# Optimization experiments

Hardware: AMD Instinct MI355X
Metric: run time of the kernel (lower is better)

The kernel has to match this reference:

```python
import jax, jax.numpy as jnp
import numpy as np

B, S, HID = 1, 4096, 2048
H, KV, D = 16, 8, 128
EPS = 1e-6
ROPE_THETA = 10000.0


def _rms_norm(x, w, eps=EPS):
    # x: [..., D], normalize over last dim in fp32 like Qwen3 RMSNorm
    xf = x.astype(jnp.float32)
    var = jnp.mean(xf * xf, axis=-1, keepdims=True)
    return (xf * jax.lax.rsqrt(var + eps)).astype(x.dtype) * w


def _rotate_half(x):
    x1, x2 = jnp.split(x, 2, axis=-1)
    return jnp.concatenate([-x2, x1], axis=-1)


def setup_inputs() -> dict:
    key = jax.random.key(0)
    ks = jax.random.split(key, 6)
    hidden_states = jax.random.normal(ks[0], (B, S, HID), dtype=jnp.float32)
    wq = jax.random.normal(ks[1], (H * D, HID), dtype=jnp.float32) * 0.02
    wk = jax.random.normal(ks[2], (KV * D, HID), dtype=jnp.float32) * 0.02
    wv = jax.random.normal(ks[3], (KV * D, HID), dtype=jnp.float32) * 0.02
    wo = jax.random.normal(ks[4], (HID, H * D), dtype=jnp.float32) * 0.02
    q_norm_w = jnp.ones((D,), dtype=jnp.float32)
    k_norm_w = jnp.ones((D,), dtype=jnp.float32)
    # real rotary tables: inv_freq over half dim, duplicated (HF convention)
    inv_freq = 1.0 / (ROPE_THETA ** (jnp.arange(0, D, 2, dtype=jnp.float32) / D))
    pos = jnp.arange(S, dtype=jnp.float32)
    freqs = pos[:, None] * inv_freq[None, :]          # [S, D/2]
    emb = jnp.concatenate([freqs, freqs], axis=-1)    # [S, D]
    cos = jnp.cos(emb)[None].astype(jnp.float32)      # [B, S, D]
    sin = jnp.sin(emb)[None].astype(jnp.float32)
    return {"hidden_states": hidden_states, "cos": cos, "sin": sin,
            "wq": wq, "wk": wk, "wv": wv, "wo": wo,
            "q_norm_w": q_norm_w, "k_norm_w": k_norm_w}


def reference(hidden_states, cos, sin, wq, wk, wv, wo, q_norm_w, k_norm_w):
    b, s, _ = hidden_states.shape
    scaling = D ** -0.5
    # QKV projections (no bias), reshape to heads, QK RMSNorm, then [b, h, s, d]
    q = _rms_norm(jnp.einsum('bsh,oh->bso', hidden_states, wq).reshape(b, s, H, D), q_norm_w)
    k = _rms_norm(jnp.einsum('bsh,oh->bso', hidden_states, wk).reshape(b, s, KV, D), k_norm_w)
    v = jnp.einsum('bsh,oh->bso', hidden_states, wv).reshape(b, s, KV, D)
    q = q.transpose(0, 2, 1, 3)  # [b, H, s, d]
    k = k.transpose(0, 2, 1, 3)  # [b, KV, s, d]
    v = v.transpose(0, 2, 1, 3)
    # RoPE (cos/sin broadcast over head dim)
    c = cos[:, None, :, :]
    sn = sin[:, None, :, :]
    q = q * c + _rotate_half(q) * sn
    k = k * c + _rotate_half(k) * sn
    # GQA: repeat KV heads to H
    groups = H // KV
    k = jnp.repeat(k, groups, axis=1)
    v = jnp.repeat(v, groups, axis=1)
    # eager causal attention, softmax in fp32
    scores = jnp.einsum('bhqd,bhkd->bhqk', q, k) * scaling
    causal = jnp.tril(jnp.ones((s, s), dtype=bool))
    scores = jnp.where(causal[None, None], scores, jnp.finfo(jnp.float32).min)
    attn = jax.nn.softmax(scores.astype(jnp.float32), axis=-1).astype(q.dtype)
    out = jnp.einsum('bhqk,bhkd->bhqd', attn, v)
    out = out.transpose(0, 2, 1, 3).reshape(b, s, H * D)
    return jnp.einsum('bso,ho->bsh', out, wo)
```

## Files before the change

kernel.cpp:

```cpp
#include <hip/hip_runtime.h>
#include <hip/hip_bf16.h>

typedef __hip_bfloat16 bf16;
typedef __attribute__((ext_vector_type(8))) short short8;
typedef __attribute__((ext_vector_type(4))) float f32x4;

#define S_LEN 4096
#define HID_DIM 2048

#define QSCALE ((float)(0.08838834764831845 * 1.4426950408889634))

__device__ __forceinline__ void gld_lds16(const void* g, void* l) {
  __builtin_amdgcn_global_load_lds(
      (const __attribute__((address_space(1))) void*)g,
      (__attribute__((address_space(3))) void*)l, 16, 0, 0);
}

__device__ __forceinline__ float fexp2(float x) {
  return __builtin_amdgcn_exp2f(x);
}

template <int CTRL>
__device__ __forceinline__ float dppf(float x) {
  return __builtin_bit_cast(
      float, __builtin_amdgcn_update_dpp(0, __builtin_bit_cast(int, x), CTRL,
                                         0xf, 0xf, true));
}
__device__ __forceinline__ float rmax16(float x) {
  x = fmaxf(x, dppf<0xB1>(x));
  x = fmaxf(x, dppf<0x4E>(x));
  x = fmaxf(x, dppf<0x141>(x));
  x = fmaxf(x, dppf<0x140>(x));
  return x;
}
__device__ __forceinline__ float rsum16(float x) {
  x += dppf<0xB1>(x);
  x += dppf<0x4E>(x);
  x += dppf<0x141>(x);
  x += dppf<0x140>(x);
  return x;
}

__global__ __launch_bounds__(256) void k_cvt(const float* __restrict__ src,
                                             bf16* __restrict__ dst, int n) {
  long i = ((long)blockIdx.x * 256 + threadIdx.x) * 8;
  if (i >= n) return;
  float4 a = *reinterpret_cast<const float4*>(src + i);
  float4 b = *reinterpret_cast<const float4*>(src + i + 4);
  float v[8] = {a.x, a.y, a.z, a.w, b.x, b.y, b.z, b.w};
  short8 o;
#pragma unroll
  for (int j = 0; j < 8; ++j) {
    bf16 h = __float2bfloat16(v[j]);
    o[j] = *reinterpret_cast<short*>(&h);
  }
  *reinterpret_cast<short8*>(dst + i) = o;
}

template <typename OutT>
__global__ __launch_bounds__(512, 1) void k_gemm256(
    const bf16* __restrict__ A, const bf16* __restrict__ B,
    OutT* __restrict__ C, int M, int N, int K) {
  __shared__ bf16 Al[2][256 * 64];
  __shared__ bf16 Bl[2][256 * 64];
  const int tid = threadIdx.x;
  const int lane = tid & 63;
  const int wid = tid >> 6;
  const int wr = wid >> 2;
  const int wc = wid & 3;
  const long brow = (long)blockIdx.y * 256;
  const long bcol = (long)blockIdx.x * 256;
  const int NT = K >> 6;

  auto stage = [&](int kt, int buf) {
    const bf16* At = A + brow * K + kt * 64;
    const bf16* Bt = B + bcol * K + kt * 64;
#pragma unroll
    for (int i = 0; i < 4; ++i) {
      const int ch = tid + i * 512;
      const int row = ch >> 3;
      const int j = (ch & 7) ^ (row & 7);
      gld_lds16(At + (size_t)row * K + j * 8, &Al[buf][(wid * 64 + i * 512) * 8]);
    }
#pragma unroll
    for (int i = 0; i < 4; ++i) {
      const int ch = tid + i * 512;
      const int row = ch >> 3;
      const int j = (ch & 7) ^ (row & 7);
      gld_lds16(Bt + (size_t)row * K + j * 8, &Bl[buf][(wid * 64 + i * 512) * 8]);
    }
  };

  f32x4 acc0[4][4], acc1[4][4];
#pragma unroll
  for (int m = 0; m < 4; ++m)
#pragma unroll
    for (int n = 0; n < 4; ++n) {
      acc0[m][n] = (f32x4){0.f, 0.f, 0.f, 0.f};
      acc1[m][n] = (f32x4){0.f, 0.f, 0.f, 0.f};
    }

  const int l15 = lane & 15;
  const int cp0 = ((lane >> 4) ^ (lane & 7)) * 8;
  const int cp1 = ((4 + (lane >> 4)) ^ (lane & 7)) * 8;

  stage(0, 0);
  stage(1, 1);
  asm volatile("s_waitcnt vmcnt(8)" ::: "memory");
  __builtin_amdgcn_s_barrier();

  for (int kt = 0; kt < NT; ++kt) {
    const bf16* Ab = &Al[kt & 1][0];
    const bf16* Bb = &Bl[kt & 1][0];
    short8 bB[4][2], aA[4][2];
#pragma unroll
    for (int n = 0; n < 4; ++n) {
      const int rb = (wc * 64 + n * 16 + l15) * 64;
      bB[n][0] = *reinterpret_cast<const short8*>(&Bb[rb + cp0]);
      bB[n][1] = *reinterpret_cast<const short8*>(&Bb[rb + cp1]);
    }
#pragma unroll
    for (int m = 0; m < 4; ++m) {
      const int ra = (wr * 128 + m * 16 + l15) * 64;
      aA[m][0] = *reinterpret_cast<const short8*>(&Ab[ra + cp0]);
      aA[m][1] = *reinterpret_cast<const short8*>(&Ab[ra + cp1]);
    }
    __builtin_amdgcn_s_setprio(1);
#pragma unroll
    for (int m = 0; m < 4; ++m)
#pragma unroll
      for (int n = 0; n < 4; ++n) {
        acc0[m][n] = __builtin_amdgcn_mfma_f32_16x16x32_bf16(aA[m][0], bB[n][0],
                                                             acc0[m][n], 0, 0, 0);
        acc0[m][n] = __builtin_amdgcn_mfma_f32_16x16x32_bf16(aA[m][1], bB[n][1],
                                                             acc0[m][n], 0, 0, 0);
      }
    __builtin_amdgcn_s_setprio(0);
#pragma unroll
    for (int m = 0; m < 4; ++m) {
      const int ra = (wr * 128 + 64 + m * 16 + l15) * 64;
      aA[m][0] = *reinterpret_cast<const short8*>(&Ab[ra + cp0]);
      aA[m][1] = *reinterpret_cast<const short8*>(&Ab[ra + cp1]);
    }
    __builtin_amdgcn_s_setprio(1);
#pragma unroll
    for (int m = 0; m < 4; ++m)
#pragma unroll
      for (int n = 0; n < 4; ++n) {
        acc1[m][n] = __builtin_amdgcn_mfma_f32_16x16x32_bf16(aA[m][0], bB[n][0],
                                                             acc1[m][n], 0, 0, 0);
        acc1[m][n] = __builtin_amdgcn_mfma_f32_16x16x32_bf16(aA[m][1], bB[n][1],
                                                             acc1[m][n], 0, 0, 0);
      }
    __builtin_amdgcn_s_setprio(0);

    if (kt + 1 < NT) {
      __builtin_amdgcn_s_barrier();
      if (kt + 2 < NT) {
        stage(kt + 2, kt & 1);
        asm volatile("s_waitcnt vmcnt(8)" ::: "memory");
      } else {
        asm volatile("s_waitcnt vmcnt(0)" ::: "memory");
      }
      __builtin_amdgcn_s_barrier();
    }
  }

#pragma unroll
  for (int mh = 0; mh < 2; ++mh) {
#pragma unroll
    for (int m = 0; m < 4; ++m) {
      const long r0 = brow + wr * 128 + mh * 64 + m * 16 + (lane >> 4) * 4;
#pragma unroll
      for (int n = 0; n < 4; ++n) {
        const long c0 = bcol + wc * 64 + n * 16 + l15;
        const f32x4 v = mh ? acc1[m][n] : acc0[m][n];
#pragma unroll
        for (int r = 0; r < 4; ++r) {
          if constexpr (sizeof(OutT) == 2)
            C[(r0 + r) * N + c0] = __float2bfloat16(v[r]);
          else
            C[(r0 + r) * N + c0] = v[r];
        }
      }
    }
  }
}

template <typename OutT>
__global__ __launch_bounds__(256) void k_gemm_bt(
    const bf16* __restrict__ A, const bf16* __restrict__ B,
    OutT* __restrict__ C, int M, int N, int K) {
  __shared__ bf16 Al[2][128 * 32];
  __shared__ bf16 Bl[2][128 * 32];
  const int tid = threadIdx.x;
  const int lane = tid & 63;
  const int wid = tid >> 6;
  const int wr = wid >> 1;
  const int wc = wid & 1;
  const long brow = (long)blockIdx.y * 128;
  const long bcol = (long)blockIdx.x * 128;
  const int rsub = lane >> 2;
  const int ksub = (lane & 3) * 8;

  f32x4 acc[4][4];
#pragma unroll
  for (int i = 0; i < 4; ++i)
#pragma unroll
    for (int j = 0; j < 4; ++j) acc[i][j] = (f32x4){0.f, 0.f, 0.f, 0.f};

  const int NT = K >> 5;

  auto stage = [&](int buf, int kt) {
    const long k0 = (long)kt << 5;
#pragma unroll
    for (int ci = 0; ci < 2; ++ci) {
      const int c = wid + ci * 4;
      gld_lds16(A + (brow + c * 16 + rsub) * K + k0 + ksub, &Al[buf][c * 512]);
      gld_lds16(B + (bcol + c * 16 + rsub) * K + k0 + ksub, &Bl[buf][c * 512]);
    }
  };

  stage(0, 0);
  __syncthreads();

  const int arow = wr * 64 + (lane & 15);
  const int nrow = wc * 64 + (lane & 15);
  const int kk = (lane >> 4) * 8;

  for (int t = 0; t < NT; ++t) {
    const int buf = t & 1;
    if (t + 1 < NT) stage(buf ^ 1, t + 1);
    short8 af[4], bfr[4];
#pragma unroll
    for (int mt = 0; mt < 4; ++mt)
      af[mt] = *reinterpret_cast<const short8*>(&Al[buf][(arow + mt * 16) * 32 + kk]);
#pragma unroll
    for (int nt = 0; nt < 4; ++nt)
      bfr[nt] = *reinterpret_cast<const short8*>(&Bl[buf][(nrow + nt * 16) * 32 + kk]);
#pragma unroll
    for (int mt = 0; mt < 4; ++mt)
#pragma unroll
      for (int nt = 0; nt < 4; ++nt)
        acc[mt][nt] = __builtin_amdgcn_mfma_f32_16x16x32_bf16(af[mt], bfr[nt],
                                                              acc[mt][nt], 0, 0, 0);
    __syncthreads();
  }

#pragma unroll
  for (int mt = 0; mt < 4; ++mt) {
    const long r0 = brow + wr * 64 + mt * 16 + (lane >> 4) * 4;
#pragma unroll
    for (int nt = 0; nt < 4; ++nt) {
      const long c0 = bcol + wc * 64 + nt * 16 + (lane & 15);
#pragma unroll
      for (int r = 0; r < 4; ++r) {
        if constexpr (sizeof(OutT) == 2)
          C[(r0 + r) * N + c0] = __float2bfloat16(acc[mt][nt][r]);
        else
          C[(r0 + r) * N + c0] = acc[mt][nt][r];
      }
    }
  }
}

__global__ __launch_bounds__(256) void k_normrope(
    const bf16* __restrict__ QKVb, const float* __restrict__ cosb,
    const float* __restrict__ sinb, const float* __restrict__ qw,
    const float* __restrict__ kw, bf16* __restrict__ Qb, bf16* __restrict__ Kb,
    bf16* __restrict__ Vb) {
  const int lane = threadIdx.x & 63;
  const int row = blockIdx.x * 4 + (threadIdx.x >> 6);
  const int s = row >> 5;
  const int idx = row & 31;
  const bf16* src = QKVb + (size_t)s * 4096 + idx * 128;
  float x0 = __bfloat162float(src[lane]);
  float x1 = __bfloat162float(src[lane + 64]);
  if (idx < 24) {
    float ss = x0 * x0 + x1 * x1;
#pragma unroll
    for (int off = 1; off < 64; off <<= 1) ss += __shfl_xor(ss, off);
    const float rn = rsqrtf(ss * (1.f / 128.f) + 1e-6f);
    const float* w = (idx < 16) ? qw : kw;
    x0 = x0 * rn * w[lane];
    x1 = x1 * rn * w[lane + 64];
    const float c0 = cosb[(size_t)s * 128 + lane];
    const float c1 = cosb[(size_t)s * 128 + lane + 64];
    const float s0 = sinb[(size_t)s * 128 + lane];
    const float s1 = sinb[(size_t)s * 128 + lane + 64];
    float o0 = x0 * c0 - x1 * s0;
    float o1 = x1 * c1 + x0 * s1;
    if (idx < 16) { o0 *= QSCALE; o1 *= QSCALE; }
    bf16* dst = (idx < 16) ? (Qb + ((size_t)idx * S_LEN + s) * 128)
                           : (Kb + ((size_t)(idx - 16) * S_LEN + s) * 128);
    dst[lane] = __float2bfloat16(o0);
    dst[lane + 64] = __float2bfloat16(o1);
  } else {
    bf16* dst = Vb + ((size_t)(idx - 24) * S_LEN + s) * 128;
    dst[lane] = __float2bfloat16(x0);
    dst[lane + 64] = __float2bfloat16(x1);
  }
}

__global__ __launch_bounds__(256) void k_vt(const bf16* __restrict__ Vb,
                                            bf16* __restrict__ Vt) {
  __shared__ bf16 Lds[64][136];
  const int tid = threadIdx.x;
  const int s0 = blockIdx.x * 64;
  const int kv = blockIdx.y;
#pragma unroll
  for (int pass = 0; pass < 4; ++pass) {
    const int c = tid + pass * 256;
    const int r = c >> 4;
    const int off = (c & 15) * 8;
    *reinterpret_cast<short8*>(&Lds[r][off]) =
        *reinterpret_cast<const short8*>(
            &Vb[((size_t)kv * S_LEN + s0 + r) * 128 + off]);
  }
  __syncthreads();
#pragma unroll
  for (int pass = 0; pass < 4; ++pass) {
    const int c = tid + pass * 256;
    const int d = c >> 3;
    const int so = (c & 7) * 8;
    short8 o;
#pragma unroll
    for (int j = 0; j < 8; ++j) {
      bf16 e = Lds[so + j][d];
      o[j] = *reinterpret_cast<short*>(&e);
    }
    *reinterpret_cast<short8*>(&Vt[((size_t)kv * 128 + d) * S_LEN + s0 + so]) = o;
  }
}

__global__ __launch_bounds__(512) void k_attn(const bf16* __restrict__ Qb,
                                              const bf16* __restrict__ Kb,
                                              const bf16* __restrict__ Vt_g,
                                              bf16* __restrict__ AO) {
  __shared__ bf16 Kl[2][64 * 128];
  __shared__ bf16 Vl[2][128 * 64];
  __shared__ bf16 Pl[4][16 * 72];
  const int tid = threadIdx.x;
  const int lane = tid & 63;
  const int wv = tid >> 6;
  const int h = blockIdx.y;
  const int kvh = h >> 1;
  const int c16 = lane & 15;
  const int kk = (lane >> 4) * 8;

  const bf16* Kbase = Kb + (size_t)kvh * S_LEN * 128;
  const bf16* Vbase = Vt_g + (size_t)kvh * 128 * S_LEN;

  auto stage = [&](int t, int buf) {
    const bf16* Kt = Kbase + (size_t)t * 64 * 128;
    const bf16* Vt = Vbase + t * 64;
#pragma unroll
    for (int p = 0; p < 4; ++p) {
      const int ch = tid + p * 256;
      const int row = ch >> 4, cp = ch & 15;
      const int c = (cp & 8) | ((cp & 7) ^ (row & 7));
      gld_lds16(Kt + row * 128 + c * 8, &Kl[buf][(wv * 64 + p * 256) * 8]);
    }
#pragma unroll
    for (int p = 0; p < 4; ++p) {
      const int ch = tid + p * 256;
      const int d = ch >> 3, cp = ch & 7;
      const int c = cp ^ (d & 7);
      gld_lds16(Vt + (size_t)d * S_LEN + c * 8, &Vl[buf][(wv * 64 + p * 256) * 8]);
    }
  };

  for (int half = 0; half < 2; ++half) {
    const int qt = half ? (63 - blockIdx.x) : blockIdx.x;
    const int qrow = qt * 64 + wv * 16;

    __syncthreads();
    stage(0, 0);

    short8 qf[4];
    {
      const bf16* qp = Qb + ((size_t)h * S_LEN + qrow + c16) * 128 + kk;
#pragma unroll
      for (int ks = 0; ks < 4; ++ks)
        qf[ks] = *reinterpret_cast<const short8*>(qp + ks * 32);
    }

    f32x4 oacc[8];
#pragma unroll
    for (int i = 0; i < 8; ++i) oacc[i] = (f32x4){0.f, 0.f, 0.f, 0.f};
    float m_run[4] = {-1e30f, -1e30f, -1e30f, -1e30f};
    float l_run[4] = {0.f, 0.f, 0.f, 0.f};

    auto tile = [&](int t, int buf, bool mask) {
      f32x4 sacc[4];
#pragma unroll
      for (int nt = 0; nt < 4; ++nt) sacc[nt] = (f32x4){0.f, 0.f, 0.f, 0.f};
#pragma unroll
      for (int ks = 0; ks < 4; ++ks) {
#pragma unroll
        for (int nt = 0; nt < 4; ++nt) {
          const int row = nt * 16 + c16;
          const int ck = ks * 4 + (lane >> 4);
          const int ckp = (ck & 8) | ((ck & 7) ^ (row & 7));
          short8 kf =
              *reinterpret_cast<const short8*>(&Kl[buf][row * 128 + ckp * 8]);
          sacc[nt] = __builtin_amdgcn_mfma_f32_16x16x32_bf16(qf[ks], kf,
                                                             sacc[nt], 0, 0, 0);
        }
      }

#pragma unroll
      for (int r = 0; r < 4; ++r) {
        const int grow = qrow + (lane >> 4) * 4 + r;
        float tm = -1e30f;
#pragma unroll
        for (int nt = 0; nt < 4; ++nt) {
          float sv = sacc[nt][r];
          if (mask && (t * 64 + nt * 16 + c16 > grow)) sv = -1e30f;
          sacc[nt][r] = sv;
          tm = fmaxf(tm, sv);
        }
        tm = rmax16(tm);
        if (__any(tm > m_run[r] + 8.f)) {
          const float mn = fmaxf(m_run[r], tm);
          const float alpha = fexp2(m_run[r] - mn);
          m_run[r] = mn;
          l_run[r] *= alpha;
#pragma unroll
          for (int dn = 0; dn < 8; ++dn) oacc[dn][r] *= alpha;
        }
        float rs = 0.f;
#pragma unroll
        for (int nt = 0; nt < 4; ++nt) {
          const float p = fexp2(sacc[nt][r] - m_run[r]);
          sacc[nt][r] = p;
          rs += p;
        }
        l_run[r] += rsum16(rs);
      }

#pragma unroll
      for (int r = 0; r < 4; ++r)
#pragma unroll
        for (int nt = 0; nt < 4; ++nt)
          Pl[wv][((lane >> 4) * 4 + r) * 72 + nt * 16 + c16] =
              __float2bfloat16(sacc[nt][r]);

#pragma unroll
      for (int ks = 0; ks < 2; ++ks) {
        short8 pf =
            *reinterpret_cast<const short8*>(&Pl[wv][c16 * 72 + ks * 32 + kk]);
#pragma unroll
        for (int dn = 0; dn < 8; ++dn) {
          const int d = dn * 16 + c16;
          const int cv = ks * 4 + (lane >> 4);
          const int cvp = cv ^ (d & 7);
          short8 vf =
              *reinterpret_cast<const short8*>(&Vl[buf][d * 64 + cvp * 8]);
          oacc[dn] =
              __builtin_amdgcn_mfma_f32_16x16x32_bf16(pf, vf, oacc[dn], 0, 0, 0);
        }
      }
    };

    __syncthreads();
    int cur = 0;
    for (int t = 0; t < qt; ++t) {
      stage(t + 1, cur ^ 1);
      tile(t, cur, false);
      __syncthreads();
      cur ^= 1;
    }
    tile(qt, cur, true);

#pragma unroll
    for (int r = 0; r < 4; ++r) {
      const float inv = 1.f / l_run[r];
      const size_t row = (size_t)(qrow + (lane >> 4) * 4 + r);
#pragma unroll
      for (int dn = 0; dn < 8; ++dn)
        AO[row * HID_DIM + h * 128 + dn * 16 + c16] =
            __float2bfloat16(oacc[dn][r] * inv);
    }
  }
}

extern "C" void kernel_launch(void* const* d_in, const int* in_sizes, int n_in,
                              void* d_out, int out_size, void* d_ws,
                              size_t ws_size, hipStream_t stream) {
  (void)in_sizes; (void)n_in; (void)out_size; (void)ws_size;
  const float* hs = (const float*)d_in[0];
  const float* cosb = (const float*)d_in[1];
  const float* sinb = (const float*)d_in[2];
  const float* wq = (const float*)d_in[3];
  const float* wk = (const float*)d_in[4];
  const float* wv = (const float*)d_in[5];
  const float* wo = (const float*)d_in[6];
  const float* qnw = (const float*)d_in[7];
  const float* knw = (const float*)d_in[8];
  float* out = (float*)d_out;
  char* ws = (char*)d_ws;

  bf16* Ah = (bf16*)(ws + 0);
  bf16* Wqkv = (bf16*)(ws + 16777216);
  bf16* Wo = (bf16*)(ws + 33554432);
  bf16* QKVb = (bf16*)(ws + 41943040);
  bf16* Qb = (bf16*)(ws + 75497472);
  bf16* Kb = (bf16*)(ws + 92274688);
  bf16* Vb = (bf16*)(ws + 100663296);
  bf16* AO = (bf16*)(ws + 109051904);
  bf16* Vt = (bf16*)(ws + 125829120);

  auto cvt = [&](const float* s, bf16* d, long n) {
    k_cvt<<<dim3((unsigned)((n / 8 + 255) / 256)), dim3(256), 0, stream>>>(
        s, d, (int)n);
  };
  cvt(hs, Ah, (long)S_LEN * HID_DIM);
  cvt(wq, Wqkv, (long)2048 * 2048);
  cvt(wk, Wqkv + (long)2048 * 2048, (long)1024 * 2048);
  cvt(wv, Wqkv + (long)3072 * 2048, (long)1024 * 2048);
  cvt(wo, Wo, (long)2048 * 2048);

  k_gemm256<bf16><<<dim3(16, 16), dim3(512), 0, stream>>>(Ah, Wqkv, QKVb, 4096,
                                                          4096, 2048);
  k_normrope<<<dim3(32768), dim3(256), 0, stream>>>(QKVb, cosb, sinb, qnw, knw,
                                                    Qb, Kb, Vb);
  k_vt<<<dim3(64, 8), dim3(256), 0, stream>>>(Vb, Vt);
  k_attn<<<dim3(32, 16), dim3(256), 0, stream>>>(Qb, Kb, Vt, AO);
  k_gemm_bt<float><<<dim3(16, 32), dim3(256), 0, stream>>>(AO, Wo, out, 4096,
                                                           2048, 2048);
}
```

Before: 308.4 us.

## Transpose attention MFMAs so each lane owns one query row in softmax

Swaps the MFMA operands for both QK^T and PV, so the score and output accumulators come out transposed. Each lane now holds a single query row. The row max and sum need only two cross-lane shuffles per tile, with one running max per lane, instead of four DPP reduction chains per row. P is written to LDS with packed bf16 conversion in an XOR-swizzled layout with no padding. The output is stored as packed bf16 pairs. The launch bound drops to 256 threads, which lets the compiler allocate more registers per thread. This adds some shuffle latency and depends on the new swizzle avoiding LDS bank conflicts.

```diff
diff --git a/kernel.cpp b/kernel.cpp
--- a/kernel.cpp
+++ b/kernel.cpp
@@ -20,25 +20,10 @@
   return __builtin_amdgcn_exp2f(x);
 }
 
-template <int CTRL>
-__device__ __forceinline__ float dppf(float x) {
-  return __builtin_bit_cast(
-      float, __builtin_amdgcn_update_dpp(0, __builtin_bit_cast(int, x), CTRL,
-                                         0xf, 0xf, true));
-}
-__device__ __forceinline__ float rmax16(float x) {
-  x = fmaxf(x, dppf<0xB1>(x));
-  x = fmaxf(x, dppf<0x4E>(x));
-  x = fmaxf(x, dppf<0x141>(x));
-  x = fmaxf(x, dppf<0x140>(x));
-  return x;
-}
-__device__ __forceinline__ float rsum16(float x) {
-  x += dppf<0xB1>(x);
-  x += dppf<0x4E>(x);
-  x += dppf<0x141>(x);
-  x += dppf<0x140>(x);
-  return x;
+__device__ __forceinline__ unsigned cvtpk_bf16(float lo, float hi) {
+  unsigned r;
+  asm("v_cvt_pk_bf16_f32 %0, %1, %2" : "=v"(r) : "v"(lo), "v"(hi));
+  return r;
 }
 
 __global__ __launch_bounds__(256) void k_cvt(const float* __restrict__ src,
@@ -333,20 +318,21 @@
   }
 }
 
-__global__ __launch_bounds__(512) void k_attn(const bf16* __restrict__ Qb,
+__global__ __launch_bounds__(256) void k_attn(const bf16* __restrict__ Qb,
                                               const bf16* __restrict__ Kb,
                                               const bf16* __restrict__ Vt_g,
                                               bf16* __restrict__ AO) {
   __shared__ bf16 Kl[2][64 * 128];
   __shared__ bf16 Vl[2][128 * 64];
-  __shared__ bf16 Pl[4][16 * 72];
+  __shared__ bf16 Pl[4][16 * 64];
   const int tid = threadIdx.x;
   const int lane = tid & 63;
   const int wv = tid >> 6;
   const int h = blockIdx.y;
   const int kvh = h >> 1;
   const int c16 = lane & 15;
-  const int kk = (lane >> 4) * 8;
+  const int hi = lane >> 4;
+  const int kk = hi * 8;
 
   const bf16* Kbase = Kb + (size_t)kvh * S_LEN * 128;
   const bf16* Vbase = Vt_g + (size_t)kvh * 128 * S_LEN;
@@ -373,6 +359,7 @@
   for (int half = 0; half < 2; ++half) {
     const int qt = half ? (63 - blockIdx.x) : blockIdx.x;
     const int qrow = qt * 64 + wv * 16;
+    const int grow = qrow + c16;
 
     __syncthreads();
     stage(0, 0);
@@ -388,8 +375,8 @@
     f32x4 oacc[8];
 #pragma unroll
     for (int i = 0; i < 8; ++i) oacc[i] = (f32x4){0.f, 0.f, 0.f, 0.f};
-    float m_run[4] = {-1e30f, -1e30f, -1e30f, -1e30f};
-    float l_run[4] = {0.f, 0.f, 0.f, 0.f};
+    float m_run = -1e30f;
+    float l_part = 0.f;
 
     auto tile = [&](int t, int buf, bool mask) {
       f32x4 sacc[4];
@@ -400,65 +387,64 @@
 #pragma unroll
         for (int nt = 0; nt < 4; ++nt) {
           const int row = nt * 16 + c16;
-          const int ck = ks * 4 + (lane >> 4);
+          const int ck = ks * 4 + hi;
           const int ckp = (ck & 8) | ((ck & 7) ^ (row & 7));
           short8 kf =
               *reinterpret_cast<const short8*>(&Kl[buf][row * 128 + ckp * 8]);
-          sacc[nt] = __builtin_amdgcn_mfma_f32_16x16x32_bf16(qf[ks], kf,
+          sacc[nt] = __builtin_amdgcn_mfma_f32_16x16x32_bf16(kf, qf[ks],
                                                              sacc[nt], 0, 0, 0);
         }
       }
 
-#pragma unroll
-      for (int r = 0; r < 4; ++r) {
-        const int grow = qrow + (lane >> 4) * 4 + r;
-        float tm = -1e30f;
-#pragma unroll
-        for (int nt = 0; nt < 4; ++nt) {
+      float tm = -1e30f;
+#pragma unroll
+      for (int nt = 0; nt < 4; ++nt)
+#pragma unroll
+        for (int r = 0; r < 4; ++r) {
           float sv = sacc[nt][r];
-          if (mask && (t * 64 + nt * 16 + c16 > grow)) sv = -1e30f;
+          if (mask && (t * 64 + nt * 16 + 4 * hi + r > grow)) sv = -1e30f;
           sacc[nt][r] = sv;
           tm = fmaxf(tm, sv);
         }
-        tm = rmax16(tm);
-        if (__any(tm > m_run[r] + 8.f)) {
-          const float mn = fmaxf(m_run[r], tm);
-          const float alpha = fexp2(m_run[r] - mn);
-          m_run[r] = mn;
-          l_run[r] *= alpha;
-#pragma unroll
-          for (int dn = 0; dn < 8; ++dn) oacc[dn][r] *= alpha;
-        }
-        float rs = 0.f;
-#pragma unroll
-        for (int nt = 0; nt < 4; ++nt) {
-          const float p = fexp2(sacc[nt][r] - m_run[r]);
-          sacc[nt][r] = p;
-          rs += p;
-        }
-        l_run[r] += rsum16(rs);
-      }
-
-#pragma unroll
-      for (int r = 0; r < 4; ++r)
-#pragma unroll
-        for (int nt = 0; nt < 4; ++nt)
-          Pl[wv][((lane >> 4) * 4 + r) * 72 + nt * 16 + c16] =
-              __float2bfloat16(sacc[nt][r]);
+      tm = fmaxf(tm, __shfl_xor(tm, 16));
+      tm = fmaxf(tm, __shfl_xor(tm, 32));
+      if (__any(tm > m_run + 8.f)) {
+        const float mn = fmaxf(m_run, tm);
+        const float alpha = fexp2(m_run - mn);
+        m_run = mn;
+        l_part *= alpha;
+#pragma unroll
+        for (int dn = 0; dn < 8; ++dn) oacc[dn] *= alpha;
+      }
+
+#pragma unroll
+      for (int nt = 0; nt < 4; ++nt) {
+        const float p0 = fexp2(sacc[nt][0] - m_run);
+        const float p1 = fexp2(sacc[nt][1] - m_run);
+        const float p2 = fexp2(sacc[nt][2] - m_run);
+        const float p3 = fexp2(sacc[nt][3] - m_run);
+        l_part += (p0 + p1) + (p2 + p3);
+        const unsigned w0 = cvtpk_bf16(p0, p1);
+        const unsigned w1 = cvtpk_bf16(p2, p3);
+        const int chunk = (2 * nt + (hi >> 1)) ^ (c16 & 7);
+        const int base = c16 * 64 + chunk * 8 + 4 * (hi & 1);
+        *reinterpret_cast<unsigned*>(&Pl[wv][base]) = w0;
+        *reinterpret_cast<unsigned*>(&Pl[wv][base + 2]) = w1;
+      }
 
 #pragma unroll
       for (int ks = 0; ks < 2; ++ks) {
+        const int pc = (ks * 4 + hi) ^ (c16 & 7);
         short8 pf =
-            *reinterpret_cast<const short8*>(&Pl[wv][c16 * 72 + ks * 32 + kk]);
+            *reinterpret_cast<const short8*>(&Pl[wv][c16 * 64 + pc * 8]);
 #pragma unroll
         for (int dn = 0; dn < 8; ++dn) {
           const int d = dn * 16 + c16;
-          const int cv = ks * 4 + (lane >> 4);
-          const int cvp = cv ^ (d & 7);
+          const int cvp = (ks * 4 + hi) ^ (d & 7);
           short8 vf =
               *reinterpret_cast<const short8*>(&Vl[buf][d * 64 + cvp * 8]);
           oacc[dn] =
-              __builtin_amdgcn_mfma_f32_16x16x32_bf16(pf, vf, oacc[dn], 0, 0, 0);
+              __builtin_amdgcn_mfma_f32_16x16x32_bf16(vf, pf, oacc[dn], 0, 0, 0);
         }
       }
     };
@@ -473,14 +459,19 @@
     }
     tile(qt, cur, true);
 
-#pragma unroll
-    for (int r = 0; r < 4; ++r) {
-      const float inv = 1.f / l_run[r];
-      const size_t row = (size_t)(qrow + (lane >> 4) * 4 + r);
-#pragma unroll
-      for (int dn = 0; dn < 8; ++dn)
-        AO[row * HID_DIM + h * 128 + dn * 16 + c16] =
-            __float2bfloat16(oacc[dn][r] * inv);
+    float lt = l_part;
+    lt += __shfl_xor(lt, 16);
+    lt += __shfl_xor(lt, 32);
+    const float inv = 1.f / lt;
+    bf16* dst = AO + (size_t)grow * HID_DIM + h * 128;
+#pragma unroll
+    for (int dn = 0; dn < 8; ++dn) {
+#pragma unroll
+      for (int w = 0; w < 2; ++w) {
+        const unsigned pk = cvtpk_bf16(oacc[dn][2 * w] * inv,
+                                       oacc[dn][2 * w + 1] * inv);
+        *reinterpret_cast<unsigned*>(&dst[dn * 16 + 4 * hi + 2 * w]) = pk;
+      }
     }
   }
 }
```

Result: faster. 287.9 us (-6.7%).
